# Optimization experiments

Hardware: AMD Instinct MI355X
Metric: run time of the kernel (lower is better)

The kernel has to match this reference:

```python
import jax, jax.numpy as jnp
import numpy as np
import math

HIDDEN = 2048
N_HEADS = 16
HEAD = HIDDEN // N_HEADS
B, S = 2, 2048


def setup_inputs() -> dict:
    key = jax.random.key(0)
    k1, k2, k3 = jax.random.split(key, 3)
    scale = 1.0 / math.sqrt(HIDDEN)
    return {
        "x": jax.random.normal(k1, (B, S, HIDDEN), dtype=jnp.float32),
        "w_qkv": jax.random.normal(k2, (HIDDEN, 3 * HIDDEN), dtype=jnp.float32) * scale,
        "b_qkv": jnp.zeros((3 * HIDDEN,), dtype=jnp.float32),
        "w_out": jax.random.normal(k3, (HIDDEN, HIDDEN), dtype=jnp.float32) * scale,
        "b_out": jnp.zeros((HIDDEN,), dtype=jnp.float32),
    }


def reference(x, w_qkv, b_qkv, w_out, b_out):
    b, s, _ = x.shape
    qkv = x @ w_qkv + b_qkv                      # [b, s, 3*hidden]
    q, k, v = jnp.split(qkv, 3, axis=-1)
    # 'b n (h l) -> b h n l'
    def heads(t):
        return t.reshape(b, s, N_HEADS, HEAD).transpose(0, 2, 1, 3)
    q, k, v = heads(q), heads(k), heads(v)
    scores = jnp.einsum("bhql,bhkl->bhqk", q, k) / math.sqrt(HEAD)
    # causal mask: positions where q_ind < k_ind get -10000 (matches source)
    q_ind = jnp.arange(s)[:, None]
    k_ind = jnp.arange(s)[None, :]
    scores = jnp.where(q_ind < k_ind, jnp.float32(-10000.0), scores)
    probs = jax.nn.softmax(scores, axis=-1)
    combined = jnp.einsum("bhqk,bhkl->bhql", probs, v)
    # 'b h q l -> b q (h l)'
    combined = combined.transpose(0, 2, 1, 3).reshape(b, s, HIDDEN)
    return combined @ w_out + b_out
```

## Files before the change

kernel.cpp:

```cpp
#include <hip/hip_runtime.h>
#include <hip/hip_bf16.h>

typedef __attribute__((ext_vector_type(4))) float f32x4;
typedef __attribute__((ext_vector_type(16))) float f32x16;
typedef __attribute__((ext_vector_type(8))) short bf16x8;

#define GBL_AS(p) (const __attribute__((address_space(1))) void*)(p)
#define LDS_AS(p) (__attribute__((address_space(3))) void*)(p)

__device__ __forceinline__ void gload_lds16(const void* g, void* l) {
  __builtin_amdgcn_global_load_lds(GBL_AS(g), LDS_AS(l), 16, 0, 0);
}

__device__ __forceinline__ ushort f2bf(float f) {
  union { float f; unsigned int u; } v; v.f = f;
  unsigned int r = v.u + 0x7fffu + ((v.u >> 16) & 1u);
  return (ushort)(r >> 16);
}

__global__ void cast_f32_bf16_kernel(const float4* __restrict__ in,
                                     ushort4* __restrict__ out, int n4) {
  int i = blockIdx.x * 256 + threadIdx.x;
  if (i < n4) {
    float4 v = in[i];
    ushort4 o;
    o.x = f2bf(v.x); o.y = f2bf(v.y); o.z = f2bf(v.z); o.w = f2bf(v.w);
    out[i] = o;
  }
}

__global__ void transpose_cast_kernel(const float* __restrict__ in,
                                      ushort* __restrict__ out, int R, int C) {
  __shared__ float tile[64][65];
  int tx = threadIdx.x & 63, ty = threadIdx.x >> 6;
  int r0 = blockIdx.y * 64, c0 = blockIdx.x * 64;
#pragma unroll
  for (int i = 0; i < 64; i += 4)
    tile[ty + i][tx] = in[(size_t)(r0 + ty + i) * C + (c0 + tx)];
  __syncthreads();
#pragma unroll
  for (int i = 0; i < 64; i += 4)
    out[(size_t)(c0 + ty + i) * R + (r0 + tx)] = f2bf(tile[tx][ty + i]);
}

template <int MODE>
__global__ __launch_bounds__(256, 2) void gemm_bt_kernel(
    const ushort* __restrict__ A, const ushort* __restrict__ Bt,
    const float* __restrict__ bias, float* __restrict__ C,
    ushort* __restrict__ Qo, ushort* __restrict__ Ko, ushort* __restrict__ Vo,
    int M, int N, int K) {
  __shared__ ushort As[128 * 64];
  __shared__ ushort Bs[128 * 64];
  const int tid = threadIdx.x;
  const int w = tid >> 6, l = tid & 63;
  const int wr = w >> 1, wc = w & 1;
  const int m0 = blockIdx.y * 128, n0 = blockIdx.x * 128;

  f32x4 acc[4][4] = {};

  const int lr = l >> 3;
  const int lc = (l & 7) ^ lr;

  for (int k0 = 0; k0 < K; k0 += 64) {
#pragma unroll
    for (int i = 0; i < 4; ++i) {
      int row = i * 32 + w * 8 + lr;
      gload_lds16(A + (size_t)(m0 + row) * K + k0 + lc * 8,
                  (char*)As + (i * 32 + w * 8) * 128);
      gload_lds16(Bt + (size_t)(n0 + row) * K + k0 + lc * 8,
                  (char*)Bs + (i * 32 + w * 8) * 128);
    }
    __syncthreads();
    const char* Ab = (const char*)As;
    const char* Bb = (const char*)Bs;
#pragma unroll
    for (int ks = 0; ks < 2; ++ks) {
      bf16x8 af[4], bfr[4];
      int cc = ks * 4 + (l >> 4);
#pragma unroll
      for (int mi = 0; mi < 4; ++mi) {
        int row = wr * 64 + mi * 16 + (l & 15);
        af[mi] = *(const bf16x8*)(Ab + row * 128 + ((cc ^ (row & 7)) << 4));
      }
#pragma unroll
      for (int ni = 0; ni < 4; ++ni) {
        int row = wc * 64 + ni * 16 + (l & 15);
        bfr[ni] = *(const bf16x8*)(Bb + row * 128 + ((cc ^ (row & 7)) << 4));
      }
#pragma unroll
      for (int mi = 0; mi < 4; ++mi)
#pragma unroll
        for (int ni = 0; ni < 4; ++ni)
          acc[mi][ni] = __builtin_amdgcn_mfma_f32_16x16x32_bf16(
              af[mi], bfr[ni], acc[mi][ni], 0, 0, 0);
    }
    __syncthreads();
  }

  if (MODE == 0) {
#pragma unroll
    for (int mi = 0; mi < 4; ++mi) {
      int row = m0 + wr * 64 + mi * 16 + ((l >> 4) << 2);
#pragma unroll
      for (int ni = 0; ni < 4; ++ni) {
        int col = n0 + wc * 64 + ni * 16 + (l & 15);
        float b = bias[col];
#pragma unroll
        for (int r = 0; r < 4; ++r)
          C[(size_t)(row + r) * N + col] = acc[mi][ni][r] + b;
      }
    }
  } else {
    const float qscale = 0.08838834764831845f * 1.4426950408889634f;
#pragma unroll
    for (int ni = 0; ni < 4; ++ni) {
      int n = n0 + wc * 64 + ni * 16 + (l & 15);
      int which = n >> 11;
      int cc2 = n & 2047;
      int h = cc2 >> 7, d = cc2 & 127;
      float b = bias[n];
#pragma unroll
      for (int mi = 0; mi < 4; ++mi) {
        int m = m0 + wr * 64 + mi * 16 + ((l >> 4) << 2);
        int bb = m >> 11, s = m & 2047;
        int bh = bb * 16 + h;
        if (which == 0) {
#pragma unroll
          for (int r = 0; r < 4; ++r)
            Qo[((size_t)bh * 2048 + s + r) * 128 + d] =
                f2bf((acc[mi][ni][r] + b) * qscale);
        } else if (which == 1) {
#pragma unroll
          for (int r = 0; r < 4; ++r)
            Ko[((size_t)bh * 2048 + s + r) * 128 + d] = f2bf(acc[mi][ni][r] + b);
        } else {
          ushort4 pk;
          pk.x = f2bf(acc[mi][ni][0] + b);
          pk.y = f2bf(acc[mi][ni][1] + b);
          pk.z = f2bf(acc[mi][ni][2] + b);
          pk.w = f2bf(acc[mi][ni][3] + b);
          *(ushort4*)(Vo + ((size_t)bh * 128 + d) * 2048 + s) = pk;
        }
      }
    }
  }
}

__global__ __launch_bounds__(512, 2) void attn_kernel(
    const ushort* __restrict__ Qg, const ushort* __restrict__ Kg,
    const ushort* __restrict__ Vtg, ushort* __restrict__ Og) {
  constexpr int S = 2048, D = 128;
  __shared__ ushort Kl[2][128 * 128];
  __shared__ ushort Vl[2][128 * 128];

  const int tid = threadIdx.x, w = tid >> 6, l = tid & 63;
  const int lid = blockIdx.x;
  const int bh = lid & 31;
  const int j = lid >> 5;
  const int g = w >> 2, wv = w & 3;
  const int qb = (g == 0) ? (8 + j) : (7 - j);
  const int wq0 = qb * 128 + wv * 32;
  const int nt_blk = 9 + j;
  const int ql = l & 31, h32 = l >> 5;

  const ushort* Qb = Qg + (size_t)bh * S * D;
  const ushort* Kb = Kg + (size_t)bh * S * D;
  const ushort* Vb = Vtg + (size_t)bh * D * S;

  bf16x8 qf[8];
#pragma unroll
  for (int ks = 0; ks < 8; ++ks)
    qf[ks] = *(const bf16x8*)(Qb + (size_t)(wq0 + ql) * D + ks * 16 + h32 * 8);

  f32x16 o[4];
#pragma unroll
  for (int dt = 0; dt < 4; ++dt) o[dt] = 0.f;
  float mrun = -1e30f, lrun = 0.f;

  auto stage = [&](int t, int buf) {
    const int k0 = t * 128;
#pragma unroll
    for (int s2 = 0; s2 < 4; ++s2) {
      int i = w * 4 + s2;
      int row = i * 4 + (l >> 4);
      int ck = (l & 15) ^ (row & 7);
      gload_lds16(Kb + (size_t)(k0 + row) * D + ck * 8,
                  (char*)Kl[buf] + i * 1024);
    }
#pragma unroll
    for (int s2 = 0; s2 < 4; ++s2) {
      int i = w * 4 + s2;
      int row = i * 4 + (l >> 4);
      int ck = (l & 15) ^ (row & 7);
      gload_lds16(Vb + (size_t)row * S + k0 + ck * 8,
                  (char*)Vl[buf] + i * 1024);
    }
  };

  stage(0, 0);

  for (int t = 0; t < nt_blk; ++t) {
    const int cur = t & 1;
    const int k0 = t * 128;
    if (t + 1 < nt_blk) {
      stage(t + 1, cur ^ 1);
      asm volatile("s_waitcnt vmcnt(8)" ::: "memory");
    } else {
      asm volatile("s_waitcnt vmcnt(0)" ::: "memory");
    }
    __builtin_amdgcn_s_barrier();

    if (k0 < wq0 + 32) {
      const char* Kc = (const char*)Kl[cur];
      const char* Vc = (const char*)Vl[cur];
      const int swz0 = ql & 7;

      f32x16 sa[4];
#pragma unroll
      for (int kt = 0; kt < 4; ++kt) sa[kt] = 0.f;
#pragma unroll
      for (int p = 0; p < 2; ++p) {
        bf16x8 kf0[8], kf1[8];
        const char* base0 = Kc + (p * 64 + ql) * 256;
        const char* base1 = Kc + (p * 64 + 32 + ql) * 256;
#pragma unroll
        for (int ks = 0; ks < 8; ++ks) {
          int c = 2 * ks + h32;
          kf0[ks] = *(const bf16x8*)(base0 + ((c ^ swz0) << 4));
          kf1[ks] = *(const bf16x8*)(base1 + ((c ^ swz0) << 4));
        }
        __builtin_amdgcn_s_setprio(1);
#pragma unroll
        for (int ks = 0; ks < 8; ++ks) {
          sa[p * 2] = __builtin_amdgcn_mfma_f32_32x32x16_bf16(
              kf0[ks], qf[ks], sa[p * 2], 0, 0, 0);
          sa[p * 2 + 1] = __builtin_amdgcn_mfma_f32_32x32x16_bf16(
              kf1[ks], qf[ks], sa[p * 2 + 1], 0, 0, 0);
        }
        __builtin_amdgcn_s_setprio(0);
      }

      if (k0 + 127 > wq0) {
        int qq = wq0 + ql;
#pragma unroll
        for (int kt = 0; kt < 4; ++kt) {
          int kb = k0 + kt * 32 + 4 * h32;
#pragma unroll
          for (int rr = 0; rr < 16; ++rr) {
            int kk = kb + (rr & 3) + 8 * (rr >> 2);
            if (qq < kk) sa[kt][rr] = -1e9f;
          }
        }
      }

      float tmax = -1e30f;
#pragma unroll
      for (int kt = 0; kt < 4; ++kt)
#pragma unroll
        for (int rr = 0; rr < 16; ++rr) tmax = fmaxf(tmax, sa[kt][rr]);
      tmax = fmaxf(tmax, __shfl_xor(tmax, 32));

      if (!__all(tmax <= mrun + 11.5f)) {
        float mnew = fmaxf(mrun, tmax);
        float e = __builtin_amdgcn_exp2f(mrun - mnew);
        lrun *= e;
        mrun = mnew;
#pragma unroll
        for (int dt = 0; dt < 4; ++dt) o[dt] *= e;
      }

      float rsum = 0.f;
#pragma unroll
      for (int kt = 0; kt < 4; ++kt)
#pragma unroll
        for (int rr = 0; rr < 16; ++rr) {
          float p = __builtin_amdgcn_exp2f(sa[kt][rr] - mrun);
          sa[kt][rr] = p;
          rsum += p;
        }
      rsum += __shfl_xor(rsum, 32);
      lrun += rsum;

#pragma unroll
      for (int kt = 0; kt < 4; ++kt) {
#pragma unroll
        for (int u2 = 0; u2 < 2; ++u2) {
          int c = 4 * kt + 2 * u2 + h32;
          bf16x8 vf[4];
#pragma unroll
          for (int dt = 0; dt < 4; ++dt) {
            int row = dt * 32 + ql;
            vf[dt] = *(const bf16x8*)(Vc + row * 256 + ((c ^ swz0) << 4));
          }
          int A0, B0, A1, B1;
          asm("v_cvt_pk_bf16_f32 %0, %1, %2"
              : "=v"(A0) : "v"(sa[kt][u2 * 8 + 0]), "v"(sa[kt][u2 * 8 + 1]));
          asm("v_cvt_pk_bf16_f32 %0, %1, %2"
              : "=v"(B0) : "v"(sa[kt][u2 * 8 + 2]), "v"(sa[kt][u2 * 8 + 3]));
          asm("v_cvt_pk_bf16_f32 %0, %1, %2"
              : "=v"(A1) : "v"(sa[kt][u2 * 8 + 4]), "v"(sa[kt][u2 * 8 + 5]));
          asm("v_cvt_pk_bf16_f32 %0, %1, %2"
              : "=v"(B1) : "v"(sa[kt][u2 * 8 + 6]), "v"(sa[kt][u2 * 8 + 7]));
          auto r02 = __builtin_amdgcn_permlane32_swap(A0, A1, false, false);
          auto r13 = __builtin_amdgcn_permlane32_swap(B0, B1, false, false);
          union { int i[4]; bf16x8 v; } pu;
          pu.i[0] = r02[0];
          pu.i[1] = r13[0];
          pu.i[2] = r02[1];
          pu.i[3] = r13[1];
          __builtin_amdgcn_s_setprio(1);
#pragma unroll
          for (int dt = 0; dt < 4; ++dt)
            o[dt] = __builtin_amdgcn_mfma_f32_32x32x16_bf16(vf[dt], pu.v, o[dt],
                                                            0, 0, 0);
          __builtin_amdgcn_s_setprio(0);
        }
      }
    }
    asm volatile("s_waitcnt lgkmcnt(0)" ::: "memory");
    __builtin_amdgcn_s_barrier();
  }

  const int b = bh >> 4, h = bh & 15;
  float inv = 1.0f / lrun;
  size_t rowbase = ((size_t)b * 2048 + (wq0 + ql)) * 2048 + h * 128;
#pragma unroll
  for (int dt = 0; dt < 4; ++dt)
#pragma unroll
    for (int r4 = 0; r4 < 4; ++r4) {
      int col = dt * 32 + r4 * 8 + h32 * 4;
      ushort4 pk;
      pk.x = f2bf(o[dt][r4 * 4 + 0] * inv);
      pk.y = f2bf(o[dt][r4 * 4 + 1] * inv);
      pk.z = f2bf(o[dt][r4 * 4 + 2] * inv);
      pk.w = f2bf(o[dt][r4 * 4 + 3] * inv);
      *(ushort4*)(Og + rowbase + col) = pk;
    }
}

extern "C" void kernel_launch(void* const* d_in, const int* in_sizes, int n_in,
                              void* d_out, int out_size, void* d_ws,
                              size_t ws_size, hipStream_t stream) {
  const float* x = (const float*)d_in[0];
  const float* w_qkv = (const float*)d_in[1];
  const float* b_qkv = (const float*)d_in[2];
  const float* w_out = (const float*)d_in[3];
  const float* b_out = (const float*)d_in[4];
  float* out = (float*)d_out;
  char* ws = (char*)d_ws;

  if (ws_size < 92274688u) return;
  ushort* xb = (ushort*)(ws);
  ushort* wqkvt = (ushort*)(ws + 16777216);
  ushort* Q = (ushort*)(ws + 41943040);
  ushort* Kb = (ushort*)(ws + 58720256);
  ushort* Vt = (ushort*)(ws + 75497472);
  ushort* comb = xb;
  ushort* woutt = wqkvt;

  cast_f32_bf16_kernel<<<8192, 256, 0, stream>>>((const float4*)x, (ushort4*)xb,
                                                 2097152);
  transpose_cast_kernel<<<dim3(96, 32), 256, 0, stream>>>(w_qkv, wqkvt, 2048,
                                                          6144);
  gemm_bt_kernel<1><<<dim3(48, 32), 256, 0, stream>>>(
      xb, wqkvt, b_qkv, nullptr, Q, Kb, Vt, 4096, 6144, 2048);
  transpose_cast_kernel<<<dim3(32, 32), 256, 0, stream>>>(w_out, woutt, 2048,
                                                          2048);
  attn_kernel<<<dim3(256), 512, 0, stream>>>(Q, Kb, Vt, comb);
  gemm_bt_kernel<0><<<dim3(16, 32), 256, 0, stream>>>(
      comb, woutt, b_out, out, nullptr, nullptr, nullptr, 4096, 2048, 2048);
}
```

Before: 223.3 us.

## Add 8-wave double-buffered QKV GEMM with interleaved MFMA and prefetch

Replaces the QKV projection GEMM with a new 512-thread kernel using 128x256 tiles, a double-buffered LDS pipeline with direct global-to-LDS loads, fine-grained barriers that interleave MFMA quadrants with next-tile staging, s_setprio around MFMA bursts, and a block-index swizzle for L2 locality. The intent is to hide global load latency and raise MFMA utilization in the largest GEMM. The old templated GEMM is reduced to the output-projection path only. The hand-tuned waitcnt and barrier schedule carries some risk of correctness or occupancy problems from the larger LDS footprint.

```diff
diff --git a/kernel.cpp b/kernel.cpp
--- a/kernel.cpp
+++ b/kernel.cpp
@@ -43,12 +43,158 @@
     out[(size_t)(c0 + ty + i) * R + (r0 + tx)] = f2bf(tile[tx][ty + i]);
 }
 
-template <int MODE>
+__global__ __launch_bounds__(512, 2) void gemm8p_kernel(
+    const ushort* __restrict__ A, const ushort* __restrict__ Bt,
+    const float* __restrict__ bias, ushort* __restrict__ Qo,
+    ushort* __restrict__ Ko, ushort* __restrict__ Vo, int M, int N, int K) {
+  __shared__ char lds[2][49152];
+
+  const int tid = threadIdx.x;
+  const int w = tid >> 6, l = tid & 63;
+  const int wm = w >> 2, wn = w & 3;
+  const int l15 = l & 15, l4 = l >> 4;
+  const int lr = l >> 3, lc = (l & 7) ^ lr;
+
+  const int bid = blockIdx.x;
+  const int swz = (bid & 7) * 96 + (bid >> 3);
+  const int by = swz & 31, bx = swz >> 5;
+  const int m0 = by * 128, n0 = bx * 256;
+
+  f32x4 acc[4][4] = {};
+  const int NT = K >> 6;
+
+  auto stageA = [&](int t, int h) {
+    int row = h * 64 + w * 8 + lr;
+    gload_lds16(A + (size_t)(m0 + row) * K + t * 64 + lc * 8,
+                lds[t & 1] + h * 8192 + w * 1024);
+  };
+  auto stageB = [&](int t, int h) {
+#pragma unroll
+    for (int s = 0; s < 2; ++s) {
+      int i = w * 2 + s;
+      int row = h * 128 + i * 8 + lr;
+      gload_lds16(Bt + (size_t)(n0 + row) * K + t * 64 + lc * 8,
+                  lds[t & 1] + 16384 + h * 16384 + i * 1024);
+    }
+  };
+
+  auto rdA2 = [&](bf16x8* a, int buf, int mi0) {
+    const char* Ab = lds[buf] + wm * 8192;
+#pragma unroll
+    for (int mi = 0; mi < 2; ++mi) {
+      int row = (mi0 + mi) * 16 + l15;
+      int sw = row & 7;
+#pragma unroll
+      for (int ks = 0; ks < 2; ++ks) {
+        int c = ks * 4 + l4;
+        a[mi * 2 + ks] = *(const bf16x8*)(Ab + row * 128 + ((c ^ sw) << 4));
+      }
+    }
+  };
+  auto rdB2 = [&](bf16x8* b, int buf, int ni0) {
+    const char* Bb = lds[buf] + 16384 + (wn >> 1) * 16384;
+#pragma unroll
+    for (int ni = 0; ni < 2; ++ni) {
+      int row = (wn & 1) * 64 + (ni0 + ni) * 16 + l15;
+      int sw = row & 7;
+#pragma unroll
+      for (int ks = 0; ks < 2; ++ks) {
+        int c = ks * 4 + l4;
+        b[ni * 2 + ks] = *(const bf16x8*)(Bb + row * 128 + ((c ^ sw) << 4));
+      }
+    }
+  };
+  auto quad8 = [&](const bf16x8* a, const bf16x8* b, int mi0, int ni0) {
+    __builtin_amdgcn_s_setprio(1);
+#pragma unroll
+    for (int mi = 0; mi < 2; ++mi)
+#pragma unroll
+      for (int ni = 0; ni < 2; ++ni)
+#pragma unroll
+        for (int ks = 0; ks < 2; ++ks)
+          acc[mi0 + mi][ni0 + ni] = __builtin_amdgcn_mfma_f32_16x16x32_bf16(
+              a[mi * 2 + ks], b[ni * 2 + ks], acc[mi0 + mi][ni0 + ni], 0, 0, 0);
+    __builtin_amdgcn_s_setprio(0);
+  };
+
+#define BAR __builtin_amdgcn_s_barrier()
+#define LGKM0 asm volatile("s_waitcnt lgkmcnt(0)" ::: "memory")
+
+  stageB(0, 0); stageA(0, 0); stageA(0, 1); stageB(0, 1);
+  stageB(1, 0); stageA(1, 0); stageA(1, 1); stageB(1, 1);
+  asm volatile("s_waitcnt vmcnt(6)" ::: "memory");
+  BAR;
+
+  for (int i2 = 0; i2 < (NT >> 1); ++i2) {
+    const int ta = 2 * i2, tb = ta + 1;
+    const bool sA = ta + 2 < NT, sB = tb + 2 < NT;
+    bf16x8 aa[4], b01[4], b23[4];
+
+    rdA2(aa, 0, 0); rdB2(b01, 0, 0);
+    BAR; LGKM0; quad8(aa, b01, 0, 0); BAR;
+    rdB2(b23, 0, 2);
+    BAR; LGKM0; quad8(aa, b23, 0, 2); BAR;
+    rdA2(aa, 0, 2);
+    if (sA) stageB(ta + 2, 0);
+    BAR; LGKM0; quad8(aa, b01, 2, 0); BAR;
+    if (sA) { stageA(ta + 2, 0); stageA(ta + 2, 1); }
+    if (sA) asm volatile("s_waitcnt vmcnt(4)" ::: "memory");
+    else    asm volatile("s_waitcnt vmcnt(0)" ::: "memory");
+    BAR; LGKM0; quad8(aa, b23, 2, 2); BAR;
+    rdA2(aa, 1, 0); rdB2(b01, 1, 0);
+    if (sA) stageB(ta + 2, 1);
+    BAR; LGKM0; quad8(aa, b01, 0, 0); BAR;
+    rdB2(b23, 1, 2);
+    BAR; LGKM0; quad8(aa, b23, 0, 2); BAR;
+    rdA2(aa, 1, 2);
+    if (sB) stageB(tb + 2, 0);
+    BAR; LGKM0; quad8(aa, b01, 2, 0); BAR;
+    if (sB) { stageB(tb + 2, 1); stageA(tb + 2, 0); stageA(tb + 2, 1); }
+    if (sB) asm volatile("s_waitcnt vmcnt(6)" ::: "memory");
+    else    asm volatile("s_waitcnt vmcnt(0)" ::: "memory");
+    BAR; LGKM0; quad8(aa, b23, 2, 2); BAR;
+  }
+#undef BAR
+#undef LGKM0
+
+  const float qscale = 0.08838834764831845f * 1.4426950408889634f;
+#pragma unroll
+  for (int ni = 0; ni < 4; ++ni) {
+    int n = n0 + wn * 64 + ni * 16 + l15;
+    int which = n >> 11;
+    int cc2 = n & 2047;
+    int h = cc2 >> 7, d = cc2 & 127;
+    float b = bias[n];
+#pragma unroll
+    for (int mi = 0; mi < 4; ++mi) {
+      int m = m0 + wm * 64 + mi * 16 + (l4 << 2);
+      int bb = m >> 11, s = m & 2047;
+      int bh = bb * 16 + h;
+      if (which == 0) {
+#pragma unroll
+        for (int r = 0; r < 4; ++r)
+          Qo[((size_t)bh * 2048 + s + r) * 128 + d] =
+              f2bf((acc[mi][ni][r] + b) * qscale);
+      } else if (which == 1) {
+#pragma unroll
+        for (int r = 0; r < 4; ++r)
+          Ko[((size_t)bh * 2048 + s + r) * 128 + d] = f2bf(acc[mi][ni][r] + b);
+      } else {
+        ushort4 pk;
+        pk.x = f2bf(acc[mi][ni][0] + b);
+        pk.y = f2bf(acc[mi][ni][1] + b);
+        pk.z = f2bf(acc[mi][ni][2] + b);
+        pk.w = f2bf(acc[mi][ni][3] + b);
+        *(ushort4*)(Vo + ((size_t)bh * 128 + d) * 2048 + s) = pk;
+      }
+    }
+  }
+}
+
 __global__ __launch_bounds__(256, 2) void gemm_bt_kernel(
     const ushort* __restrict__ A, const ushort* __restrict__ Bt,
-    const float* __restrict__ bias, float* __restrict__ C,
-    ushort* __restrict__ Qo, ushort* __restrict__ Ko, ushort* __restrict__ Vo,
-    int M, int N, int K) {
+    const float* __restrict__ bias, float* __restrict__ C, int M, int N,
+    int K) {
   __shared__ ushort As[128 * 64];
   __shared__ ushort Bs[128 * 64];
   const int tid = threadIdx.x;
@@ -97,51 +243,16 @@
     __syncthreads();
   }
 
-  if (MODE == 0) {
-#pragma unroll
-    for (int mi = 0; mi < 4; ++mi) {
-      int row = m0 + wr * 64 + mi * 16 + ((l >> 4) << 2);
-#pragma unroll
-      for (int ni = 0; ni < 4; ++ni) {
-        int col = n0 + wc * 64 + ni * 16 + (l & 15);
-        float b = bias[col];
-#pragma unroll
-        for (int r = 0; r < 4; ++r)
-          C[(size_t)(row + r) * N + col] = acc[mi][ni][r] + b;
-      }
-    }
-  } else {
-    const float qscale = 0.08838834764831845f * 1.4426950408889634f;
+#pragma unroll
+  for (int mi = 0; mi < 4; ++mi) {
+    int row = m0 + wr * 64 + mi * 16 + ((l >> 4) << 2);
 #pragma unroll
     for (int ni = 0; ni < 4; ++ni) {
-      int n = n0 + wc * 64 + ni * 16 + (l & 15);
-      int which = n >> 11;
-      int cc2 = n & 2047;
-      int h = cc2 >> 7, d = cc2 & 127;
-      float b = bias[n];
-#pragma unroll
-      for (int mi = 0; mi < 4; ++mi) {
-        int m = m0 + wr * 64 + mi * 16 + ((l >> 4) << 2);
-        int bb = m >> 11, s = m & 2047;
-        int bh = bb * 16 + h;
-        if (which == 0) {
-#pragma unroll
-          for (int r = 0; r < 4; ++r)
-            Qo[((size_t)bh * 2048 + s + r) * 128 + d] =
-                f2bf((acc[mi][ni][r] + b) * qscale);
-        } else if (which == 1) {
-#pragma unroll
-          for (int r = 0; r < 4; ++r)
-            Ko[((size_t)bh * 2048 + s + r) * 128 + d] = f2bf(acc[mi][ni][r] + b);
-        } else {
-          ushort4 pk;
-          pk.x = f2bf(acc[mi][ni][0] + b);
-          pk.y = f2bf(acc[mi][ni][1] + b);
-          pk.z = f2bf(acc[mi][ni][2] + b);
-          pk.w = f2bf(acc[mi][ni][3] + b);
-          *(ushort4*)(Vo + ((size_t)bh * 128 + d) * 2048 + s) = pk;
-        }
-      }
+      int col = n0 + wc * 64 + ni * 16 + (l & 15);
+      float b = bias[col];
+#pragma unroll
+      for (int rr = 0; rr < 4; ++rr)
+        C[(size_t)(row + rr) * N + col] = acc[mi][ni][rr] + b;
     }
   }
 }
@@ -362,11 +473,11 @@
                                                  2097152);
   transpose_cast_kernel<<<dim3(96, 32), 256, 0, stream>>>(w_qkv, wqkvt, 2048,
                                                           6144);
-  gemm_bt_kernel<1><<<dim3(48, 32), 256, 0, stream>>>(
-      xb, wqkvt, b_qkv, nullptr, Q, Kb, Vt, 4096, 6144, 2048);
+  gemm8p_kernel<<<dim3(768), 512, 0, stream>>>(xb, wqkvt, b_qkv, Q, Kb, Vt,
+                                               4096, 6144, 2048);
   transpose_cast_kernel<<<dim3(32, 32), 256, 0, stream>>>(w_out, woutt, 2048,
                                                           2048);
   attn_kernel<<<dim3(256), 512, 0, stream>>>(Q, Kb, Vt, comb);
-  gemm_bt_kernel<0><<<dim3(16, 32), 256, 0, stream>>>(
-      comb, woutt, b_out, out, nullptr, nullptr, nullptr, 4096, 2048, 2048);
-}
+  gemm_bt_kernel<<<dim3(16, 32), 256, 0, stream>>>(comb, woutt, b_out, out,
+                                                   4096, 2048, 2048);
+}
```

After: 234.6 us. 1.05x slower.
